# Performance work log

Hardware: AMD Instinct MI355X
Metric: run time of the kernel (lower is better)

Reference implementation:

```python
import jax, jax.numpy as jnp
import numpy as np

N_HEADS = 16
D_HEAD = 64
MAX_POS = 128

def setup_inputs() -> dict:
    key = jax.random.key(0)
    ks = jax.random.split(key, 9)
    B, L, D = 4, 1024, 1024
    s = 0.02
    return {
        'x': jax.random.normal(ks[0], (B, L, D), jnp.float32),
        'pad_mask': jnp.ones((B, L), jnp.float32),
        'Wq': jax.random.normal(ks[1], (D, D), jnp.float32) * s,
        'bq': jnp.zeros((D,), jnp.float32),
        'Wk': jax.random.normal(ks[2], (D, D), jnp.float32) * s,
        'bk': jnp.zeros((D,), jnp.float32),
        'Wv': jax.random.normal(ks[3], (D, D), jnp.float32) * s,
        'bv': jnp.zeros((D,), jnp.float32),
        'Wo': jax.random.normal(ks[4], (D, D), jnp.float32) * s,
        'bo': jnp.zeros((D,), jnp.float32),
        'posK': jax.random.normal(ks[5], (2 * MAX_POS + 1, D_HEAD), jnp.float32) * s,
        'posV': jax.random.normal(ks[6], (2 * MAX_POS + 1, D_HEAD), jnp.float32) * s,
    }

def reference(x, pad_mask, Wq, bq, Wk, bk, Wv, bv, Wo, bo, posK, posV):
    B, L, _ = x.shape
    H, d = N_HEADS, D_HEAD
    def proj(W, b):
        y = x @ W + b                      # [B, L, H*d]
        return y.reshape(B, L, H, d).transpose(0, 2, 1, 3)  # [B, H, L, d]
    Q = proj(Wq, bq)
    K = proj(Wk, bk)
    V = proj(Wv, bv)
    # relative position index, clamped to [-MAX_POS, MAX_POS], shifted to [0, 2*MAX_POS]
    idx = jnp.arange(L)
    pos_index = jnp.clip(idx[None, :] - idx[:, None], -MAX_POS, MAX_POS) + MAX_POS  # [L, L]
    pos_emb_K = posK[pos_index]            # [L, L, d]
    pos_emb_V = posV[pos_index]            # [L, L, d]
    S1 = jnp.einsum('bhqd,bhkd->bhqk', Q, K)
    S2 = jnp.einsum('bhqd,qkd->bhqk', Q, pos_emb_K)
    S = (S1 + S2) / np.sqrt(d).astype(np.float32)
    # NOTE: original multiplies scores by the pad mask (not additive -inf)
    S = S * pad_mask[:, None, None, :]
    A = jax.nn.softmax(S, axis=-1)
    O1 = jnp.einsum('bhqk,bhkd->bhqd', A, V)
    O2 = jnp.einsum('bhqk,qkd->bhqd', A, pos_emb_V)
    out = (O1 + O2).transpose(0, 2, 1, 3).reshape(B, L, H * d)
    return out @ Wo + bo
```

## Files before the change

kernel.cpp:

```cpp
#include <hip/hip_runtime.h>
#include <math.h>

#define L_SEQ 1024
#define NB 4
#define NH 16
#define DH 64
#define BH_TOT (NB * NH)
#define GQ_TOT (BH_TOT * L_SEQ)
#define NPOS 257
#define QP_STRIDE 260
#define LDK 72
#define LDQP 72
#define LDPV 264

typedef unsigned short ushort_t;
typedef __attribute__((ext_vector_type(8))) short bf16x8;
typedef __attribute__((ext_vector_type(4))) float f32x4;

__device__ inline ushort_t f2bf_rne(float x) {
    unsigned u = __float_as_uint(x);
    unsigned r = u + 0x7FFFu + ((u >> 16) & 1u);
    return (ushort_t)(r >> 16);
}
__device__ inline float bf2f(ushort_t h) {
    return __uint_as_float(((unsigned)h) << 16);
}
__device__ inline uint4 pack8hi(float4 a0, float4 a1) {
    float v[8] = {a0.x, a0.y, a0.z, a0.w, a1.x, a1.y, a1.z, a1.w};
    unsigned hh[4];
    #pragma unroll
    for (int j = 0; j < 4; j++)
        hh[j] = (unsigned)f2bf_rne(v[2*j]) | ((unsigned)f2bf_rne(v[2*j+1]) << 16);
    return (uint4){hh[0], hh[1], hh[2], hh[3]};
}

__global__ __launch_bounds__(256)
void split_f32_hi(const float* __restrict__ A, ushort_t* __restrict__ hi)
{
    const size_t base = ((size_t)blockIdx.x * 256 + threadIdx.x) * 8;
    *(uint4*)(hi + base) =
        pack8hi(*(const float4*)(A + base), *(const float4*)(A + base + 4));
}

__global__ __launch_bounds__(256)
void split_transpose3(const float* __restrict__ Wq, const float* __restrict__ Wk,
                      const float* __restrict__ Wv, ushort_t* __restrict__ Thi,
                      ushort_t* __restrict__ Tlo)
{
    __shared__ float Ws[64][65];
    const int tid = threadIdx.x;
    const int k0 = blockIdx.x * 64;
    const int n0 = blockIdx.y * 64;
    const int z  = blockIdx.z;
    const float* W = (z == 0) ? Wq : (z == 1) ? Wk : Wv;
    ushort_t* Hh = Thi + (size_t)z * 1048576;
    ushort_t* Ll = Tlo + (size_t)z * 1048576;
    const int r  = tid >> 4;
    const int c4 = (tid & 15) * 4;
    #pragma unroll
    for (int i = 0; i < 4; i++) {
        float4 v = *(const float4*)(W + (size_t)(k0 + r + i*16) * 1024 + n0 + c4);
        Ws[r + i*16][c4+0] = v.x;
        Ws[r + i*16][c4+1] = v.y;
        Ws[r + i*16][c4+2] = v.z;
        Ws[r + i*16][c4+3] = v.w;
    }
    __syncthreads();
    #pragma unroll
    for (int i = 0; i < 4; i++) {
        const int nl = r + i*16;
        ushort_t h[4], l[4];
        #pragma unroll
        for (int j = 0; j < 4; j++) {
            float x = Ws[c4 + j][nl];
            h[j] = f2bf_rne(x);
            l[j] = f2bf_rne(x - bf2f(h[j]));
        }
        size_t off = (size_t)(n0 + nl) * 1024 + k0 + c4;
        uint2 H, L;
        H.x = (unsigned)h[0] | ((unsigned)h[1] << 16);
        H.y = (unsigned)h[2] | ((unsigned)h[3] << 16);
        L.x = (unsigned)l[0] | ((unsigned)l[1] << 16);
        L.y = (unsigned)l[2] | ((unsigned)l[3] << 16);
        *(uint2*)(Hh + off) = H;
        *(uint2*)(Ll + off) = L;
    }
}

__global__ __launch_bounds__(256)
void split_transpose(const float* __restrict__ W, ushort_t* __restrict__ Thi,
                     ushort_t* __restrict__ Tlo, int Kdim, int Ndim)
{
    __shared__ float Ws[64][65];
    const int tid = threadIdx.x;
    const int k0 = blockIdx.x * 64;
    const int n0 = blockIdx.y * 64;
    const int r  = tid >> 4;
    const int c4 = (tid & 15) * 4;
    #pragma unroll
    for (int i = 0; i < 4; i++) {
        float4 v = *(const float4*)(W + (size_t)(k0 + r + i*16) * Ndim + n0 + c4);
        Ws[r + i*16][c4+0] = v.x;
        Ws[r + i*16][c4+1] = v.y;
        Ws[r + i*16][c4+2] = v.z;
        Ws[r + i*16][c4+3] = v.w;
    }
    __syncthreads();
    #pragma unroll
    for (int i = 0; i < 4; i++) {
        const int nl = r + i*16;
        ushort_t h[4], l[4];
        #pragma unroll
        for (int j = 0; j < 4; j++) {
            float x = Ws[c4 + j][nl];
            h[j] = f2bf_rne(x);
            l[j] = f2bf_rne(x - bf2f(h[j]));
        }
        size_t off = (size_t)(n0 + nl) * Kdim + k0 + c4;
        uint2 H, L;
        H.x = (unsigned)h[0] | ((unsigned)h[1] << 16);
        H.y = (unsigned)h[2] | ((unsigned)h[3] << 16);
        L.x = (unsigned)l[0] | ((unsigned)l[1] << 16);
        L.y = (unsigned)l[2] | ((unsigned)l[3] << 16);
        *(uint2*)(Thi + off) = H;
        *(uint2*)(Tlo + off) = L;
    }
}

__global__ __launch_bounds__(256)
void prep_pvt(const float* __restrict__ posV, ushort_t* __restrict__ pvTg)
{
    __shared__ float Ws[64][65];
    const int tid = threadIdx.x;
    const int c = blockIdx.x;
    {
        const int r  = tid >> 2;
        const int d0 = (tid & 3) * 16;
        const float* src = posV + (size_t)(c * 64 + r + 1) * 64 + d0;
        #pragma unroll
        for (int i = 0; i < 4; i++) {
            float4 v = *(const float4*)(src + i * 4);
            Ws[r][d0 + i*4 + 0] = v.x;
            Ws[r][d0 + i*4 + 1] = v.y;
            Ws[r][d0 + i*4 + 2] = v.z;
            Ws[r][d0 + i*4 + 3] = v.w;
        }
    }
    __syncthreads();
    {
        const int d  = tid >> 2;
        const int r0 = (tid & 3) * 16;
        #pragma unroll
        for (int k = 0; k < 16; k++)
            pvTg[(size_t)d * LDPV + c * 64 + r0 + k] = f2bf_rne(Ws[r0 + k][d]);
    }
}

__global__ __launch_bounds__(256)
void gemm_qkv(const ushort_t* __restrict__ Ahi,
              const ushort_t* __restrict__ Bhi, const ushort_t* __restrict__ Blo,
              const float* __restrict__ bq, const float* __restrict__ bk,
              const float* __restrict__ bv,
              ushort_t* __restrict__ Qbu, ushort_t* __restrict__ Kbu,
              ushort_t* __restrict__ Vtu)
{
    __shared__ ushort_t As[64 * LDK];
    __shared__ ushort_t Bs[2][64 * LDK];
    const int tid  = threadIdx.x;
    const int m0   = blockIdx.x * 64;
    const int n0   = blockIdx.y * 64;
    const int nb   = n0 >> 10;
    const int wave = tid >> 6, lane = tid & 63;
    const int w0 = wave >> 1, w1 = wave & 1;
    const int lr = lane & 15, lq = lane >> 4;
    const int K = 1024;

    f32x4 acc[2][2];
    #pragma unroll
    for (int i = 0; i < 2; i++)
        #pragma unroll
        for (int j = 0; j < 2; j++)
            acc[i][j] = (f32x4){0.f, 0.f, 0.f, 0.f};

    for (int k0 = 0; k0 < K; k0 += 64) {
        __syncthreads();
        #pragma unroll
        for (int c = 0; c < 2; c++) {
            const int n   = c * 256 + tid;
            const int row = n >> 3;
            const int col = (n & 7) * 8;
            const size_t ga = (size_t)(m0 + row) * K + k0 + col;
            const size_t gb = (size_t)(n0 + row) * K + k0 + col;
            const int la = row * LDK + col;
            *(uint4*)&As[la]    = *(const uint4*)(Ahi + ga);
            *(uint4*)&Bs[0][la] = *(const uint4*)(Bhi + gb);
            *(uint4*)&Bs[1][la] = *(const uint4*)(Blo + gb);
        }
        __syncthreads();
        #pragma unroll
        for (int ks = 0; ks < 2; ks++) {
            bf16x8 ah[2], bh[2], bl[2];
            #pragma unroll
            for (int i = 0; i < 2; i++) {
                const int ar = (w0*32 + i*16 + lr) * LDK + ks*32 + lq*8;
                ah[i] = *(const bf16x8*)&As[ar];
                const int br = (w1*32 + i*16 + lr) * LDK + ks*32 + lq*8;
                bh[i] = *(const bf16x8*)&Bs[0][br];
                bl[i] = *(const bf16x8*)&Bs[1][br];
            }
            #pragma unroll
            for (int i = 0; i < 2; i++)
                #pragma unroll
                for (int j = 0; j < 2; j++) {
                    acc[i][j] = __builtin_amdgcn_mfma_f32_16x16x32_bf16(ah[i], bh[j], acc[i][j], 0, 0, 0);
                    acc[i][j] = __builtin_amdgcn_mfma_f32_16x16x32_bf16(ah[i], bl[j], acc[i][j], 0, 0, 0);
                }
        }
    }

    const float* bp = (nb == 0) ? bq : (nb == 1) ? bk : bv;
    ushort_t* Cout = (nb == 0) ? Qbu : (nb == 1) ? Kbu : Vtu;
    #pragma unroll
    for (int j = 0; j < 2; j++) {
        const int colg = n0 + w1*32 + j*16 + lr;
        const int c1   = colg & 1023;
        const float bcol = bp[c1];
        const int h = c1 >> 6, dd = c1 & 63;
        #pragma unroll
        for (int i = 0; i < 2; i++) {
            #pragma unroll
            for (int r = 0; r < 4; r++) {
                const int m = m0 + w0*32 + i*16 + lq*4 + r;
                const float v = acc[i][j][r] + bcol;
                const int b = m >> 10, lp = m & 1023;
                const size_t off = (nb == 2)
                    ? ((size_t)(b * NH + h) * DH + dd) * L_SEQ + lp
                    : ((size_t)(b * NH + h) * L_SEQ + lp) * DH + dd;
                Cout[off] = f2bf_rne(v);
            }
        }
    }
}

__global__ __launch_bounds__(256)
void gemm_mfma(const ushort_t* __restrict__ Ahi, const ushort_t* __restrict__ Alo,
               const ushort_t* __restrict__ Bhi, const ushort_t* __restrict__ Blo,
               const float* __restrict__ bias, float* __restrict__ C,
               int M, int N, int K)
{
    __shared__ ushort_t As[2][64 * LDK];
    __shared__ ushort_t Bs[2][64 * LDK];
    const int tid  = threadIdx.x;
    const int m0   = blockIdx.x * 64;
    const int n0   = blockIdx.y * 64;
    const int wave = tid >> 6, lane = tid & 63;
    const int w0 = wave >> 1, w1 = wave & 1;
    const int lr = lane & 15, lq = lane >> 4;

    f32x4 acc[2][2];
    #pragma unroll
    for (int i = 0; i < 2; i++)
        #pragma unroll
        for (int j = 0; j < 2; j++)
            acc[i][j] = (f32x4){0.f, 0.f, 0.f, 0.f};

    for (int k0 = 0; k0 < K; k0 += 64) {
        __syncthreads();
        #pragma unroll
        for (int c = 0; c < 2; c++) {
            const int n   = c * 256 + tid;
            const int row = n >> 3;
            const int col = (n & 7) * 8;
            const size_t ga = (size_t)(m0 + row) * K + k0 + col;
            const size_t gb = (size_t)(n0 + row) * K + k0 + col;
            const int la = row * LDK + col;
            *(uint4*)&As[0][la] = *(const uint4*)(Ahi + ga);
            *(uint4*)&As[1][la] = *(const uint4*)(Alo + ga);
            *(uint4*)&Bs[0][la] = *(const uint4*)(Bhi + gb);
            *(uint4*)&Bs[1][la] = *(const uint4*)(Blo + gb);
        }
        __syncthreads();
        #pragma unroll
        for (int ks = 0; ks < 2; ks++) {
            bf16x8 ah[2], al[2], bh[2], bl[2];
            #pragma unroll
            for (int i = 0; i < 2; i++) {
                const int ar = (w0*32 + i*16 + lr) * LDK + ks*32 + lq*8;
                ah[i] = *(const bf16x8*)&As[0][ar];
                al[i] = *(const bf16x8*)&As[1][ar];
                const int br = (w1*32 + i*16 + lr) * LDK + ks*32 + lq*8;
                bh[i] = *(const bf16x8*)&Bs[0][br];
                bl[i] = *(const bf16x8*)&Bs[1][br];
            }
            #pragma unroll
            for (int i = 0; i < 2; i++)
                #pragma unroll
                for (int j = 0; j < 2; j++) {
                    acc[i][j] = __builtin_amdgcn_mfma_f32_16x16x32_bf16(ah[i], bh[j], acc[i][j], 0, 0, 0);
                    acc[i][j] = __builtin_amdgcn_mfma_f32_16x16x32_bf16(ah[i], bl[j], acc[i][j], 0, 0, 0);
                    acc[i][j] = __builtin_amdgcn_mfma_f32_16x16x32_bf16(al[i], bh[j], acc[i][j], 0, 0, 0);
                }
        }
    }

    #pragma unroll
    for (int j = 0; j < 2; j++) {
        const int colg = n0 + w1*32 + j*16 + lr;
        const float bcol = bias[colg];
        #pragma unroll
        for (int i = 0; i < 2; i++) {
            #pragma unroll
            for (int r = 0; r < 4; r++) {
                const int m = m0 + w0*32 + i*16 + lq*4 + r;
                C[(size_t)m * N + colg] = acc[i][j][r] + bcol;
            }
        }
    }
}

__global__ __launch_bounds__(256)
void qp_mfma(const ushort_t* __restrict__ Qu, const float* __restrict__ posK,
             ushort_t* __restrict__ Qpu)
{
    const int tid = threadIdx.x;
    const size_t m0 = (size_t)blockIdx.x * 64;
    const int n0 = blockIdx.y * 64;
    const int wave = tid >> 6, lane = tid & 63;
    const int wm = (wave >> 1) * 32, wn = (wave & 1) * 32;
    const int lr = lane & 15, lq = lane >> 4;

    bf16x8 af[2][2];
    #pragma unroll
    for (int i = 0; i < 2; i++) {
        const ushort_t* qrow = Qu + (m0 + wm + i*16 + lr) * DH;
        #pragma unroll
        for (int kc = 0; kc < 2; kc++)
            af[i][kc] = *(const bf16x8*)(qrow + kc*32 + lq*8);
    }
    bf16x8 bf[2][2];
    #pragma unroll
    for (int j = 0; j < 2; j++) {
        int n = n0 + wn + j*16 + lr;
        const float* krow = posK + (size_t)(n < 256 ? n : 256) * DH;
        #pragma unroll
        for (int kc = 0; kc < 2; kc++) {
            const float* s = krow + kc*32 + lq*8;
            uint4 u = pack8hi(*(const float4*)s, *(const float4*)(s + 4));
            bf[j][kc] = *(bf16x8*)&u;
        }
    }

    f32x4 acc[2][2];
    #pragma unroll
    for (int i = 0; i < 2; i++)
        #pragma unroll
        for (int j = 0; j < 2; j++)
            acc[i][j] = (f32x4){0.f, 0.f, 0.f, 0.f};
    #pragma unroll
    for (int kc = 0; kc < 2; kc++)
        #pragma unroll
        for (int i = 0; i < 2; i++)
            #pragma unroll
            for (int j = 0; j < 2; j++)
                acc[i][j] = __builtin_amdgcn_mfma_f32_16x16x32_bf16(af[i][kc], bf[j][kc], acc[i][j], 0, 0, 0);

    #pragma unroll
    for (int i = 0; i < 2; i++)
        #pragma unroll
        for (int j = 0; j < 2; j++) {
            const int n = n0 + wn + j*16 + lr;
            if (n < NPOS) {
                #pragma unroll
                for (int r = 0; r < 4; r++) {
                    const size_t m = m0 + wm + i*16 + lq*4 + r;
                    Qpu[m * QP_STRIDE + n] = f2bf_rne(acc[i][j][r]);
                }
            }
        }
}

__global__ __launch_bounds__(256)
void attn_kernel(const ushort_t* __restrict__ Qu, const ushort_t* __restrict__ Ku,
                 const ushort_t* __restrict__ Vtu, const ushort_t* __restrict__ Qpu,
                 const float* __restrict__ pm,
                 ushort_t* __restrict__ SbandU,
                 float* __restrict__ O1a, float* __restrict__ O1b,
                 float* __restrict__ lsum2, float* __restrict__ clo2,
                 float* __restrict__ chi2)
{
    __shared__ ushort_t Ks[64 * LDK];
    __shared__ ushort_t Vs[64 * LDK];
    __shared__ ushort_t QpsP[64 * LDQP];
    __shared__ float mk[64];

    const int tid = threadIdx.x;
    const int blk = blockIdx.x;
    const int bh  = blk >> 5;
    const int qb  = (blk >> 1) & 15;
    const int ks  = blk & 1;
    const int b   = bh >> 4;
    const int q0  = qb * 64;
    const size_t gq0 = (size_t)bh * L_SEQ + q0;
    const int wave = tid >> 6, lane = tid & 63;
    const int lr = lane & 15, lq = lane >> 4;
    const int qw = wave * 16;

    const int sr0 = tid >> 3,          sc0 = (tid & 7) * 8;
    const int sr1 = (256 + tid) >> 3,  sc1 = ((256 + tid) & 7) * 8;
    const int qpRowL = qw + (lane >> 2);
    const int qpCol0 = (lane & 3) * 16;

    const ushort_t* Kg  = Ku  + (size_t)bh * (L_SEQ * DH);
    const ushort_t* Vtg = Vtu + (size_t)bh * (DH * L_SEQ);

    bf16x8 qa[2];
    {
        const ushort_t* qrow = Qu + (gq0 + qw + lr) * DH;
        #pragma unroll
        for (int kc = 0; kc < 2; kc++)
            qa[kc] = *(const bf16x8*)(qrow + kc * 32 + lq * 8);
    }

    if (ks == 0 && tid < 64) {
        const int q = q0 + tid;
        ushort_t* bandRow = SbandU + (gq0 + tid) * 256;
        for (int j = 0; j < 127 - q; j++)    bandRow[j] = 0;
        for (int j = 254; j > 1150 - q; j--) bandRow[j] = 0;
        bandRow[255] = 0;
    }

    f32x4 Oacc[4];
    #pragma unroll
    for (int j = 0; j < 4; j++) Oacc[j] = (f32x4){0.f, 0.f, 0.f, 0.f};
    float lpart[4] = {}, clpart[4] = {}, chpart[4] = {};

    uint4 kva0, kva1, kvb0, kvb1;
    ushort_t qpr[16];
    float mkr = 0.f;
    {
        const int k0 = ks * 512;
        kva0 = *(const uint4*)(Kg + (size_t)(k0 + sr0) * DH + sc0);
        kva1 = *(const uint4*)(Kg + (size_t)(k0 + sr1) * DH + sc1);
        kvb0 = *(const uint4*)(Vtg + (size_t)sr0 * L_SEQ + k0 + sc0);
        kvb1 = *(const uint4*)(Vtg + (size_t)sr1 * L_SEQ + k0 + sc1);
        const int qg = q0 + qpRowL;
        #pragma unroll
        for (int c = 0; c < 16; c++) {
            int rel = k0 + qpCol0 + c - qg;
            rel = rel < -128 ? -128 : (rel > 128 ? 128 : rel);
            qpr[c] = Qpu[(gq0 + qpRowL) * QP_STRIDE + rel + 128];
        }
        if (tid < 64) mkr = pm[b * L_SEQ + k0 + tid];
    }

    for (int t = 0; t < 8; t++) {
        const int k0 = (ks * 8 + t) * 64;
        __syncthreads();

        *(uint4*)&Ks[sr0 * LDK + sc0] = kva0;
        *(uint4*)&Ks[sr1 * LDK + sc1] = kva1;
        *(uint4*)&Vs[sr0 * LDK + sc0] = kvb0;
        *(uint4*)&Vs[sr1 * LDK + sc1] = kvb1;
        {
            ushort_t* dst = &QpsP[qpRowL * LDQP + qpCol0];
            #pragma unroll
            for (int c = 0; c < 8; c++)
                ((unsigned*)dst)[c] = (unsigned)qpr[2*c] | ((unsigned)qpr[2*c+1] << 16);
        }
        if (tid < 64) mk[tid] = mkr;
        __syncthreads();

        if (t < 7) {
            const int k0n = k0 + 64;
            kva0 = *(const uint4*)(Kg + (size_t)(k0n + sr0) * DH + sc0);
            kva1 = *(const uint4*)(Kg + (size_t)(k0n + sr1) * DH + sc1);
            kvb0 = *(const uint4*)(Vtg + (size_t)sr0 * L_SEQ + k0n + sc0);
            kvb1 = *(const uint4*)(Vtg + (size_t)sr1 * L_SEQ + k0n + sc1);
            const int qg = q0 + qpRowL;
            #pragma unroll
            for (int c = 0; c < 16; c++) {
                int rel = k0n + qpCol0 + c - qg;
                rel = rel < -128 ? -128 : (rel > 128 ? 128 : rel);
                qpr[c] = Qpu[(gq0 + qpRowL) * QP_STRIDE + rel + 128];
            }
            if (tid < 64) mkr = pm[b * L_SEQ + k0n + tid];
        }

        f32x4 Sacc[4];
        #pragma unroll
        for (int j = 0; j < 4; j++) Sacc[j] = (f32x4){0.f, 0.f, 0.f, 0.f};
        #pragma unroll
        for (int kc = 0; kc < 2; kc++) {
            #pragma unroll
            for (int j = 0; j < 4; j++) {
                bf16x8 kb = *(const bf16x8*)&Ks[(j*16 + lr) * LDK + kc*32 + lq*8];
                Sacc[j] = __builtin_amdgcn_mfma_f32_16x16x32_bf16(qa[kc], kb, Sacc[j], 0, 0, 0);
            }
        }

        ushort_t pb[4][4];
        #pragma unroll
        for (int r = 0; r < 4; r++) {
            const int ql = qw + lq*4 + r;
            const int q  = q0 + ql;
            const size_t gq = gq0 + ql;
            ushort_t* bandRow = SbandU + gq * 256 + 127;
            #pragma unroll
            for (int j = 0; j < 4; j++) {
                const int kl = j*16 + lr;
                const int k  = k0 + kl;
                const int rel = k - q;
                float s = (Sacc[j][r] + bf2f(QpsP[ql * LDQP + kl])) * 0.125f;
                s *= mk[kl];
                const float p = __expf(s);
                lpart[r] += p;
                const ushort_t ph = f2bf_rne(p);
                if (rel <= -128)      clpart[r] += p;
                else if (rel >= 128)  chpart[r] += p;
                else                  bandRow[rel] = ph;
                pb[j][r] = ph;
            }
        }

        #pragma unroll
        for (int r = 0; r < 4; r++)
            #pragma unroll
            for (int j = 0; j < 4; j++)
                QpsP[(qw + lq*4 + r) * LDQP + j*16 + lr] = pb[j][r];

        #pragma unroll
        for (int kc = 0; kc < 2; kc++) {
            bf16x8 pa = *(const bf16x8*)&QpsP[(qw + lr) * LDQP + kc*32 + lq*8];
            #pragma unroll
            for (int j = 0; j < 4; j++) {
                bf16x8 vb = *(const bf16x8*)&Vs[(j*16 + lr) * LDK + kc*32 + lq*8];
                Oacc[j] = __builtin_amdgcn_mfma_f32_16x16x32_bf16(pa, vb, Oacc[j], 0, 0, 0);
            }
        }
    }

    #pragma unroll
    for (int off = 1; off < 16; off <<= 1) {
        #pragma unroll
        for (int r = 0; r < 4; r++) {
            lpart[r]  += __shfl_xor(lpart[r],  off, 64);
            clpart[r] += __shfl_xor(clpart[r], off, 64);
            chpart[r] += __shfl_xor(chpart[r], off, 64);
        }
    }
    if (lr == 0) {
        #pragma unroll
        for (int r = 0; r < 4; r++) {
            const size_t o = (size_t)ks * GQ_TOT + gq0 + qw + lq*4 + r;
            lsum2[o] = lpart[r];
            clo2[o]  = clpart[r];
            chi2[o]  = chpart[r];
        }
    }

    float* O1o = ks ? O1b : O1a;
    #pragma unroll
    for (int j = 0; j < 4; j++)
        #pragma unroll
        for (int r = 0; r < 4; r++)
            O1o[(gq0 + qw + lq*4 + r) * DH + j*16 + lr] = Oacc[j][r];
}

__global__ __launch_bounds__(256)
void post_mfma(const ushort_t* __restrict__ SbandU, const ushort_t* __restrict__ pvTg,
               const float* __restrict__ O1a, const float* __restrict__ O1b,
               const float* __restrict__ lsum2, const float* __restrict__ clo2,
               const float* __restrict__ chi2, const float* __restrict__ posV,
               ushort_t* __restrict__ athi, ushort_t* __restrict__ atlo)
{
    __shared__ ushort_t pvT[64 * LDPV];
    const int tid = threadIdx.x;
    const size_t q0 = (size_t)blockIdx.x * 64;
    const int wave = tid >> 6, lane = tid & 63;
    const int w0 = wave >> 1, w1 = wave & 1;
    const int lr = lane & 15, lq = lane >> 4;

    {
        const unsigned* src = (const unsigned*)pvTg;
        unsigned* dst = (unsigned*)pvT;
        for (int i = tid; i < 64 * LDPV / 2; i += 256) dst[i] = src[i];
    }
    __syncthreads();

    f32x4 acc[2][2];
    #pragma unroll
    for (int i = 0; i < 2; i++)
        #pragma unroll
        for (int j = 0; j < 2; j++)
            acc[i][j] = (f32x4){0.f, 0.f, 0.f, 0.f};

    const ushort_t* bandB = SbandU + q0 * 256;
    #pragma unroll
    for (int kc = 0; kc < 8; kc++) {
        bf16x8 a[2], bv[2];
        #pragma unroll
        for (int i = 0; i < 2; i++) {
            a[i]  = *(const bf16x8*)&bandB[(size_t)(w0*32 + i*16 + lr) * 256 + kc*32 + lq*8];
            bv[i] = *(const bf16x8*)&pvT[(w1*32 + i*16 + lr) * LDPV + kc*32 + lq*8];
        }
        #pragma unroll
        for (int i = 0; i < 2; i++)
            #pragma unroll
            for (int j = 0; j < 2; j++)
                acc[i][j] = __builtin_amdgcn_mfma_f32_16x16x32_bf16(a[i], bv[j], acc[i][j], 0, 0, 0);
    }

    #pragma unroll
    for (int i = 0; i < 2; i++) {
        #pragma unroll
        for (int r = 0; r < 4; r++) {
            const int ql = w0*32 + i*16 + lq*4 + r;
            const size_t gq = q0 + ql;
            const float li = lsum2[gq] + lsum2[GQ_TOT + gq];
            const float cl = clo2[gq]  + clo2[GQ_TOT + gq];
            const float ch = chi2[gq]  + chi2[GQ_TOT + gq];
            const float inv = 1.0f / li;
            const int b  = (int)(gq >> 14);
            const int h  = (int)((gq >> 10) & 15);
            const int lp = (int)(gq & 1023);
            const size_t obase = ((size_t)(b * L_SEQ + lp) * 1024) + h * 64;
            #pragma unroll
            for (int j = 0; j < 2; j++) {
                const int dd = w1*32 + j*16 + lr;
                float o = O1a[gq * DH + dd] + O1b[gq * DH + dd] + acc[i][j][r]
                        + cl * posV[dd] + ch * posV[256 * 64 + dd];
                o *= inv;
                const ushort_t hh = f2bf_rne(o);
                const ushort_t ll = f2bf_rne(o - bf2f(hh));
                athi[obase + dd] = hh;
                atlo[obase + dd] = ll;
            }
        }
    }
}

extern "C" void kernel_launch(void* const* d_in, const int* in_sizes, int n_in,
                              void* d_out, int out_size, void* d_ws, size_t ws_size,
                              hipStream_t stream)
{
    const float* x    = (const float*)d_in[0];
    const float* pmk  = (const float*)d_in[1];
    const float* Wq   = (const float*)d_in[2];
    const float* bq   = (const float*)d_in[3];
    const float* Wk   = (const float*)d_in[4];
    const float* bk   = (const float*)d_in[5];
    const float* Wv   = (const float*)d_in[6];
    const float* bv   = (const float*)d_in[7];
    const float* Wo   = (const float*)d_in[8];
    const float* bo   = (const float*)d_in[9];
    const float* posK = (const float*)d_in[10];
    const float* posV = (const float*)d_in[11];
    float* out = (float*)d_out;

    ushort_t* u = (ushort_t*)d_ws;
    ushort_t* Qbu    = u;
    ushort_t* Kbu    = Qbu + (size_t)GQ_TOT * DH;
    ushort_t* Vtu    = Kbu + (size_t)GQ_TOT * DH;
    ushort_t* Qpu    = Vtu + (size_t)GQ_TOT * DH;
    ushort_t* SbandU = Qpu + (size_t)GQ_TOT * QP_STRIDE;
    ushort_t* athi   = SbandU + (size_t)GQ_TOT * 256;
    ushort_t* atlo   = athi + (size_t)GQ_TOT * DH;
    ushort_t* pvTg   = atlo + (size_t)GQ_TOT * DH;
    float* O1a   = (float*)(pvTg + 64 * LDPV + 64);
    float* O1b   = O1a   + (size_t)GQ_TOT * DH;
    float* lsum2 = O1b   + (size_t)GQ_TOT * DH;
    float* clo2  = lsum2 + 2 * (size_t)GQ_TOT;
    float* chi2  = clo2  + 2 * (size_t)GQ_TOT;

    ushort_t* bb    = SbandU;
    ushort_t* xhi   = bb;
    ushort_t* wqkvh = xhi + 4194304;
    ushort_t* wqkvl = wqkvh + 3145728;
    ushort_t* woh   = bb;
    ushort_t* wol   = woh + 1048576;

    dim3 gb(256);

    split_f32_hi<<<dim3(2048), gb, 0, stream>>>(x, xhi);
    split_transpose3<<<dim3(16, 16, 3), gb, 0, stream>>>(Wq, Wk, Wv, wqkvh, wqkvl);
    prep_pvt<<<dim3(4), gb, 0, stream>>>(posV, pvTg);
    gemm_qkv<<<dim3(64, 48), gb, 0, stream>>>(xhi, wqkvh, wqkvl, bq, bk, bv,
                                              Qbu, Kbu, Vtu);
    qp_mfma<<<dim3(1024, 5), gb, 0, stream>>>(Qbu, posK, Qpu);
    attn_kernel<<<dim3(2048), gb, 0, stream>>>(Qbu, Kbu, Vtu, Qpu, pmk,
                                               SbandU, O1a, O1b, lsum2, clo2, chi2);
    post_mfma<<<dim3(GQ_TOT / 64), gb, 0, stream>>>(SbandU, pvTg, O1a, O1b, lsum2,
                                                    clo2, chi2, posV, athi, atlo);
    split_transpose<<<dim3(16, 16), gb, 0, stream>>>(Wo, woh, wol, 1024, 1024);
    gemm_mfma<<<dim3(64, 16), gb, 0, stream>>>(athi, atlo, woh, wol, bo, out,
                                               4096, 1024, 1024);
}
```

Measured before the change: 380.7 us.

## Use 128x128 register-prefetched QKV GEMM tiles and store partial O1 in bf16

The QKV projection GEMM moves from 64x64 tiles to 128x128 tiles with a K-step of 32. Each wave computes a 4x4 grid of MFMA fragments, and the next K-slice is prefetched from global memory into registers while the current slice is computed. This raises data reuse per shared-memory load and overlaps load latency with MFMA work, at the cost of more registers per thread and fewer blocks. Separately, the split-K partial outputs O1a/O1b are stored as bf16 instead of fp32, halving that intermediate traffic but adding rounding error before the final normalisation.

Result: faster. 359.9 us (-5.5%).

```diff
diff --git a/kernel.cpp b/kernel.cpp
--- a/kernel.cpp
+++ b/kernel.cpp
@@ -12,6 +12,7 @@
 #define LDK 72
 #define LDQP 72
 #define LDPV 264
+#define LDK32 40
 
 typedef unsigned short ushort_t;
 typedef __attribute__((ext_vector_type(8))) short bf16x8;
@@ -157,80 +158,93 @@
 }
 
 __global__ __launch_bounds__(256)
-void gemm_qkv(const ushort_t* __restrict__ Ahi,
-              const ushort_t* __restrict__ Bhi, const ushort_t* __restrict__ Blo,
-              const float* __restrict__ bq, const float* __restrict__ bk,
-              const float* __restrict__ bv,
-              ushort_t* __restrict__ Qbu, ushort_t* __restrict__ Kbu,
-              ushort_t* __restrict__ Vtu)
-{
-    __shared__ ushort_t As[64 * LDK];
-    __shared__ ushort_t Bs[2][64 * LDK];
+void gemm_qkv128(const ushort_t* __restrict__ Ahi,
+                 const ushort_t* __restrict__ Bhi, const ushort_t* __restrict__ Blo,
+                 const float* __restrict__ bq, const float* __restrict__ bk,
+                 const float* __restrict__ bv,
+                 ushort_t* __restrict__ Qbu, ushort_t* __restrict__ Kbu,
+                 ushort_t* __restrict__ Vtu)
+{
+    __shared__ ushort_t As[128 * LDK32];
+    __shared__ ushort_t Bs[2][128 * LDK32];
     const int tid  = threadIdx.x;
-    const int m0   = blockIdx.x * 64;
-    const int n0   = blockIdx.y * 64;
+    const int m0   = blockIdx.x * 128;
+    const int n0   = blockIdx.y * 128;
     const int nb   = n0 >> 10;
     const int wave = tid >> 6, lane = tid & 63;
-    const int w0 = wave >> 1, w1 = wave & 1;
+    const int wr = wave >> 1, wc = wave & 1;
     const int lr = lane & 15, lq = lane >> 4;
     const int K = 1024;
 
-    f32x4 acc[2][2];
-    #pragma unroll
-    for (int i = 0; i < 2; i++)
-        #pragma unroll
-        for (int j = 0; j < 2; j++)
+    const int r0 = tid >> 1,        c0 = (tid & 1) * 16;
+    const int sA0 = tid,       rA0 = sA0 >> 2, cA0 = (sA0 & 3) * 8;
+    const int sA1 = 256 + tid, rA1 = sA1 >> 2, cA1 = (sA1 & 3) * 8;
+    (void)r0; (void)c0;
+
+    f32x4 acc[4][4];
+    #pragma unroll
+    for (int i = 0; i < 4; i++)
+        #pragma unroll
+        for (int j = 0; j < 4; j++)
             acc[i][j] = (f32x4){0.f, 0.f, 0.f, 0.f};
 
-    for (int k0 = 0; k0 < K; k0 += 64) {
+    uint4 pa0, pa1, pbh0, pbh1, pbl0, pbl1;
+    {
+        const size_t a0 = (size_t)(m0 + rA0) * K + cA0, a1 = (size_t)(m0 + rA1) * K + cA1;
+        const size_t b0 = (size_t)(n0 + rA0) * K + cA0, b1 = (size_t)(n0 + rA1) * K + cA1;
+        pa0  = *(const uint4*)(Ahi + a0); pa1  = *(const uint4*)(Ahi + a1);
+        pbh0 = *(const uint4*)(Bhi + b0); pbh1 = *(const uint4*)(Bhi + b1);
+        pbl0 = *(const uint4*)(Blo + b0); pbl1 = *(const uint4*)(Blo + b1);
+    }
+
+    for (int it = 0; it < 32; it++) {
         __syncthreads();
-        #pragma unroll
-        for (int c = 0; c < 2; c++) {
-            const int n   = c * 256 + tid;
-            const int row = n >> 3;
-            const int col = (n & 7) * 8;
-            const size_t ga = (size_t)(m0 + row) * K + k0 + col;
-            const size_t gb = (size_t)(n0 + row) * K + k0 + col;
-            const int la = row * LDK + col;
-            *(uint4*)&As[la]    = *(const uint4*)(Ahi + ga);
-            *(uint4*)&Bs[0][la] = *(const uint4*)(Bhi + gb);
-            *(uint4*)&Bs[1][la] = *(const uint4*)(Blo + gb);
-        }
+        *(uint4*)&As[rA0 * LDK32 + cA0]    = pa0;
+        *(uint4*)&As[rA1 * LDK32 + cA1]    = pa1;
+        *(uint4*)&Bs[0][rA0 * LDK32 + cA0] = pbh0;
+        *(uint4*)&Bs[0][rA1 * LDK32 + cA1] = pbh1;
+        *(uint4*)&Bs[1][rA0 * LDK32 + cA0] = pbl0;
+        *(uint4*)&Bs[1][rA1 * LDK32 + cA1] = pbl1;
         __syncthreads();
-        #pragma unroll
-        for (int ks = 0; ks < 2; ks++) {
-            bf16x8 ah[2], bh[2], bl[2];
-            #pragma unroll
-            for (int i = 0; i < 2; i++) {
-                const int ar = (w0*32 + i*16 + lr) * LDK + ks*32 + lq*8;
-                ah[i] = *(const bf16x8*)&As[ar];
-                const int br = (w1*32 + i*16 + lr) * LDK + ks*32 + lq*8;
-                bh[i] = *(const bf16x8*)&Bs[0][br];
-                bl[i] = *(const bf16x8*)&Bs[1][br];
-            }
-            #pragma unroll
-            for (int i = 0; i < 2; i++)
-                #pragma unroll
-                for (int j = 0; j < 2; j++) {
-                    acc[i][j] = __builtin_amdgcn_mfma_f32_16x16x32_bf16(ah[i], bh[j], acc[i][j], 0, 0, 0);
-                    acc[i][j] = __builtin_amdgcn_mfma_f32_16x16x32_bf16(ah[i], bl[j], acc[i][j], 0, 0, 0);
-                }
-        }
+        if (it < 31) {
+            const int k0 = (it + 1) * 32;
+            const size_t a0 = (size_t)(m0 + rA0) * K + k0 + cA0, a1 = (size_t)(m0 + rA1) * K + k0 + cA1;
+            const size_t b0 = (size_t)(n0 + rA0) * K + k0 + cA0, b1 = (size_t)(n0 + rA1) * K + k0 + cA1;
+            pa0  = *(const uint4*)(Ahi + a0); pa1  = *(const uint4*)(Ahi + a1);
+            pbh0 = *(const uint4*)(Bhi + b0); pbh1 = *(const uint4*)(Bhi + b1);
+            pbl0 = *(const uint4*)(Blo + b0); pbl1 = *(const uint4*)(Blo + b1);
+        }
+
+        bf16x8 ah[4], bh[4], bl[4];
+        #pragma unroll
+        for (int i = 0; i < 4; i++) {
+            ah[i] = *(const bf16x8*)&As[(wr*64 + i*16 + lr) * LDK32 + lq*8];
+            const int br = (wc*64 + i*16 + lr) * LDK32 + lq*8;
+            bh[i] = *(const bf16x8*)&Bs[0][br];
+            bl[i] = *(const bf16x8*)&Bs[1][br];
+        }
+        #pragma unroll
+        for (int i = 0; i < 4; i++)
+            #pragma unroll
+            for (int j = 0; j < 4; j++) {
+                acc[i][j] = __builtin_amdgcn_mfma_f32_16x16x32_bf16(ah[i], bh[j], acc[i][j], 0, 0, 0);
+                acc[i][j] = __builtin_amdgcn_mfma_f32_16x16x32_bf16(ah[i], bl[j], acc[i][j], 0, 0, 0);
+            }
     }
 
     const float* bp = (nb == 0) ? bq : (nb == 1) ? bk : bv;
     ushort_t* Cout = (nb == 0) ? Qbu : (nb == 1) ? Kbu : Vtu;
     #pragma unroll
-    for (int j = 0; j < 2; j++) {
-        const int colg = n0 + w1*32 + j*16 + lr;
+    for (int j = 0; j < 4; j++) {
+        const int colg = n0 + wc*64 + j*16 + lr;
         const int c1   = colg & 1023;
         const float bcol = bp[c1];
         const int h = c1 >> 6, dd = c1 & 63;
         #pragma unroll
-        for (int i = 0; i < 2; i++) {
+        for (int i = 0; i < 4; i++) {
             #pragma unroll
             for (int r = 0; r < 4; r++) {
-                const int m = m0 + w0*32 + i*16 + lq*4 + r;
+                const int m = m0 + wr*64 + i*16 + lq*4 + r;
                 const float v = acc[i][j][r] + bcol;
                 const int b = m >> 10, lp = m & 1023;
                 const size_t off = (nb == 2)
@@ -384,7 +398,7 @@
                  const ushort_t* __restrict__ Vtu, const ushort_t* __restrict__ Qpu,
                  const float* __restrict__ pm,
                  ushort_t* __restrict__ SbandU,
-                 float* __restrict__ O1a, float* __restrict__ O1b,
+                 ushort_t* __restrict__ O1a, ushort_t* __restrict__ O1b,
                  float* __restrict__ lsum2, float* __restrict__ clo2,
                  float* __restrict__ chi2)
 {
@@ -558,17 +572,17 @@
         }
     }
 
-    float* O1o = ks ? O1b : O1a;
+    ushort_t* O1o = ks ? O1b : O1a;
     #pragma unroll
     for (int j = 0; j < 4; j++)
         #pragma unroll
         for (int r = 0; r < 4; r++)
-            O1o[(gq0 + qw + lq*4 + r) * DH + j*16 + lr] = Oacc[j][r];
+            O1o[(gq0 + qw + lq*4 + r) * DH + j*16 + lr] = f2bf_rne(Oacc[j][r]);
 }
 
 __global__ __launch_bounds__(256)
 void post_mfma(const ushort_t* __restrict__ SbandU, const ushort_t* __restrict__ pvTg,
-               const float* __restrict__ O1a, const float* __restrict__ O1b,
+               const ushort_t* __restrict__ O1a, const ushort_t* __restrict__ O1b,
                const float* __restrict__ lsum2, const float* __restrict__ clo2,
                const float* __restrict__ chi2, const float* __restrict__ posV,
                ushort_t* __restrict__ athi, ushort_t* __restrict__ atlo)
@@ -627,7 +641,8 @@
             #pragma unroll
             for (int j = 0; j < 2; j++) {
                 const int dd = w1*32 + j*16 + lr;
-                float o = O1a[gq * DH + dd] + O1b[gq * DH + dd] + acc[i][j][r]
+                float o = bf2f(O1a[gq * DH + dd]) + bf2f(O1b[gq * DH + dd])
+                        + acc[i][j][r]
                         + cl * posV[dd] + ch * posV[256 * 64 + dd];
                 o *= inv;
                 const ushort_t hh = f2bf_rne(o);
@@ -665,10 +680,10 @@
     ushort_t* SbandU = Qpu + (size_t)GQ_TOT * QP_STRIDE;
     ushort_t* athi   = SbandU + (size_t)GQ_TOT * 256;
     ushort_t* atlo   = athi + (size_t)GQ_TOT * DH;
-    ushort_t* pvTg   = atlo + (size_t)GQ_TOT * DH;
-    float* O1a   = (float*)(pvTg + 64 * LDPV + 64);
-    float* O1b   = O1a   + (size_t)GQ_TOT * DH;
-    float* lsum2 = O1b   + (size_t)GQ_TOT * DH;
+    ushort_t* O1a    = atlo + (size_t)GQ_TOT * DH;
+    ushort_t* O1b    = O1a  + (size_t)GQ_TOT * DH;
+    ushort_t* pvTg   = O1b  + (size_t)GQ_TOT * DH;
+    float* lsum2 = (float*)(pvTg + 64 * LDPV + 64);
     float* clo2  = lsum2 + 2 * (size_t)GQ_TOT;
     float* chi2  = clo2  + 2 * (size_t)GQ_TOT;
 
@@ -684,8 +699,8 @@
     split_f32_hi<<<dim3(2048), gb, 0, stream>>>(x, xhi);
     split_transpose3<<<dim3(16, 16, 3), gb, 0, stream>>>(Wq, Wk, Wv, wqkvh, wqkvl);
     prep_pvt<<<dim3(4), gb, 0, stream>>>(posV, pvTg);
-    gemm_qkv<<<dim3(64, 48), gb, 0, stream>>>(xhi, wqkvh, wqkvl, bq, bk, bv,
-                                              Qbu, Kbu, Vtu);
+    gemm_qkv128<<<dim3(32, 24), gb, 0, stream>>>(xhi, wqkvh, wqkvl, bq, bk, bv,
+                                                 Qbu, Kbu, Vtu);
     qp_mfma<<<dim3(1024, 5), gb, 0, stream>>>(Qbu, posK, Qpu);
     attn_kernel<<<dim3(2048), gb, 0, stream>>>(Qbu, Kbu, Vtu, Qpu, pmk,
                                                SbandU, O1a, O1b, lsum2, clo2, chi2);
```
